# Kernel optimization log

Hardware: AMD Instinct MI355X
Metric: run time of the kernel (lower is better)

The kernel has to match this reference:

```python
import jax, jax.numpy as jnp
import numpy as np

NUM_CLASSES = 90
MAX_DET_POINTS = 5000
MAX_DET_PER_IMAGE = 100
IOU_THR = 0.5
NEG = -1e10
IMAGE_SIZE = 768


def _make_anchors(image_size=IMAGE_SIZE, min_level=3, num_levels=5, anchor_scale=4.0):
    """EfficientDet-style anchors, ordered (level, y, x, anchor-config), yxyx."""
    boxes_all = []
    for li in range(num_levels):
        stride = 2 ** (min_level + li)
        boxes_level = []
        for octave in range(3):
            for aspect in (1.0, 2.0, 0.5):
                base = anchor_scale * stride * 2.0 ** (octave / 3.0)
                ax = np.sqrt(aspect)
                half_x = base * ax / 2.0
                half_y = base / ax / 2.0
                x = np.arange(stride / 2.0, image_size, stride)
                y = np.arange(stride / 2.0, image_size, stride)
                xv, yv = np.meshgrid(x, y)  # [H, W], row-major matches NHWC flatten
                xv = xv.reshape(-1)
                yv = yv.reshape(-1)
                boxes = np.stack([yv - half_y, xv - half_x, yv + half_y, xv + half_x], axis=1)
                boxes_level.append(boxes[:, None, :])
        boxes_all.append(np.concatenate(boxes_level, axis=1).reshape(-1, 4))
    return np.concatenate(boxes_all, axis=0).astype(np.float32)


def setup_inputs() -> dict:
    key = jax.random.key(0)
    ks = jax.random.split(key, 10)
    B = 8
    hw = [96, 48, 24, 12, 6]
    inp = {}
    for i, s in enumerate(hw):
        inp[f"cls{i}"] = jax.random.normal(ks[i], (B, 810, s, s), jnp.float32)
        inp[f"box{i}"] = jax.random.normal(ks[5 + i], (B, 36, s, s), jnp.float32)
    inp["anchor_boxes"] = jnp.asarray(_make_anchors())
    return inp


def _decode_boxes(rel_codes, anchors):
    # anchors: yxyx; rel_codes: (ty, tx, th, tw) -> output xyxy
    ycenter_a = (anchors[..., 0] + anchors[..., 2]) / 2
    xcenter_a = (anchors[..., 1] + anchors[..., 3]) / 2
    ha = anchors[..., 2] - anchors[..., 0]
    wa = anchors[..., 3] - anchors[..., 1]
    ty, tx, th, tw = rel_codes[..., 0], rel_codes[..., 1], rel_codes[..., 2], rel_codes[..., 3]
    w = jnp.exp(tw) * wa
    h = jnp.exp(th) * ha
    yc = ty * ha + ycenter_a
    xc = tx * wa + xcenter_a
    return jnp.stack([xc - w / 2, yc - h / 2, xc + w / 2, yc + h / 2], axis=-1)


def _nms_indices(boxes, scores, classes, iou_thr=IOU_THR, max_out=MAX_DET_PER_IMAGE):
    """torchvision.batched_nms: class-offset boxes, greedy NMS, return idx + valid mask."""
    boxes = jax.lax.stop_gradient(boxes)
    scores = jax.lax.stop_gradient(scores)
    off = classes.astype(boxes.dtype) * (jnp.max(boxes) + 1.0)
    b = boxes + off[:, None]  # [N,4]
    area = (b[:, 2] - b[:, 0]) * (b[:, 3] - b[:, 1])

    def body(i, state):
        live, sel, val = state
        idx = jnp.argmax(live)
        ok = live[idx] > 0.0  # sigmoid scores are >0; suppressed are NEG
        bi = b[idx]
        ix = jnp.maximum(0.0, jnp.minimum(b[:, 2], bi[2]) - jnp.maximum(b[:, 0], bi[0]))
        iy = jnp.maximum(0.0, jnp.minimum(b[:, 3], bi[3]) - jnp.maximum(b[:, 1], bi[1]))
        inter = ix * iy
        iou = inter / (area + area[idx] - inter + 1e-8)
        live = jnp.where(iou > iou_thr, NEG, live).at[idx].set(NEG)
        return live, sel.at[i].set(idx), val.at[i].set(ok)

    state0 = (scores, jnp.zeros((max_out,), jnp.int32), jnp.zeros((max_out,), bool))
    _, sel, val = jax.lax.fori_loop(0, max_out, body, state0)
    return sel, val


def _forward(cls_levels, box_levels, anchor_boxes):
    B = cls_levels[0].shape[0]
    C = NUM_CLASSES
    # NCHW -> NHWC -> [B, A, C] / [B, A, 4], concat over levels
    cls_all = jnp.concatenate(
        [c.transpose(0, 2, 3, 1).reshape(B, -1, C) for c in cls_levels], axis=1)
    box_all = jnp.concatenate(
        [b.transpose(0, 2, 3, 1).reshape(B, -1, 4) for b in box_levels], axis=1)

    top_vals, top_idx = jax.lax.top_k(cls_all.reshape(B, -1), MAX_DET_POINTS)
    indices = top_idx // C  # anchor index
    classes = top_idx % C
    box_topk = jnp.take_along_axis(box_all, indices[..., None], axis=1)  # [B,K,4]
    anchors_sel = anchor_boxes[indices]  # [B,K,4]

    boxes = _decode_boxes(box_topk, anchors_sel)  # xyxy [B,K,4]
    scores = jax.nn.sigmoid(top_vals)  # [B,K]

    def per_image(bx, sc, cl):
        sel, val = _nms_indices(bx, sc, cl)
        det = jnp.concatenate(
            [bx[sel], sc[sel, None], (cl[sel] + 1).astype(bx.dtype)[:, None]], axis=1)
        return jnp.where(val[:, None], det, 0.0)  # pad invalid rows with zeros

    return jax.vmap(per_image)(boxes, scores, classes)  # [B, 100, 6]


def reference(cls0, cls1, cls2, cls3, cls4, box0, box1, box2, box3, box4, anchor_boxes):
    return _forward((cls0, cls1, cls2, cls3, cls4), (box0, box1, box2, box3, box4), anchor_boxes)
```

## Files before the change

### kernel.cpp

```cpp
#include <hip/hip_runtime.h>
#include <stdint.h>

#define KDET 5000
#define MAX_OUT 100
#define PRE_THR 2.5f
#define CAND_CAP 98304u
#define SEL_N 8192u
#define TOTAL_F 9943560u
#define STAGE_CAP 1024u
#define HBINS 2048u
#define FB 0x18040u
#define CHUNKW 512u
#define SC2_CAP 2048u
#define NMSK_CAP 4096u
#define SEL_STRIDE 5120u
#define DEC_BLKS 16u
#define DEC_PER 313u

#define WS_CNT   0
#define WS_HIST  4096
#define WS_ZERO  69632
#define WS_META  69632
#define WS_PMAX  69760
#define WS_SELG  131072
#define WS_BX    458752
#define WS_SC    1098752
#define WS_CL    1258752
#define WS_CAND  1441792

__device__ __forceinline__ unsigned f2key(float f) {
  unsigned u = __float_as_uint(f);
  return u ^ (unsigned)(((int)u >> 31) | 0x80000000);
}

__global__ __launch_bounds__(256, 8) void scan_kernel(
    const float* __restrict__ c0, const float* __restrict__ c1,
    const float* __restrict__ c2, const float* __restrict__ c3,
    const float* __restrict__ c4,
    unsigned long long* __restrict__ cand,
    unsigned* __restrict__ cnt, unsigned* __restrict__ hist)
{
  __shared__ unsigned sh_hist[HBINS];
  __shared__ unsigned long long sh_cand[STAGE_CAP];
  __shared__ unsigned sh_ccnt;
  __shared__ unsigned sh_base;

  const unsigned img = blockIdx.y;
  const unsigned tid = threadIdx.x;
  const float* ptrs[5] = {c0, c1, c2, c3, c4};
  const unsigned lvlElems[5] = {7464960u, 1866240u, 466560u, 116640u, 29160u};
  const unsigned hw2s[5] = {9216u, 2304u, 576u, 144u, 36u};
  const unsigned fbases[5] = {0u, 7464960u, 9331200u, 9797760u, 9914400u};
  unsigned long long* candI = cand + (size_t)img * CAND_CAP;
  unsigned* histI = hist + img * HBINS;

  for (unsigned b = tid; b < HBINS; b += 256u) sh_hist[b] = 0u;
  if (tid == 0) sh_ccnt = 0u;
  __syncthreads();

#pragma unroll
  for (int lev = 0; lev < 5; ++lev) {
    const float4* p = (const float4*)(ptrs[lev] + (size_t)img * lvlElems[lev]);
    const unsigned n4 = lvlElems[lev] >> 2;
    const unsigned hw2 = hw2s[lev];
    const unsigned fbase = fbases[lev];
    const unsigned chunk = 256u * 4u;
    const unsigned sweep = gridDim.x * chunk;
    for (unsigned s0 = blockIdx.x * chunk; s0 < n4; s0 += sweep) {
      float4 v[4]; unsigned idxs[4]; bool ok[4];
#pragma unroll
      for (int u = 0; u < 4; ++u) {
        idxs[u] = s0 + (unsigned)u * 256u + tid;
        ok[u] = idxs[u] < n4;
        if (ok[u]) v[u] = p[idxs[u]];
      }
#pragma unroll
      for (int u = 0; u < 4; ++u) {
        if (!ok[u]) continue;
        float vs[4] = {v[u].x, v[u].y, v[u].z, v[u].w};
#pragma unroll
        for (int j = 0; j < 4; ++j) {
          float f = vs[j];
          if (f > PRE_THR) {
            unsigned key = f2key(f);
            unsigned bin = (key >> 15) - FB;
            if (bin > HBINS - 1u) bin = HBINS - 1u;
            atomicAdd(&sh_hist[bin], 1u);
            unsigned linear = idxs[u] * 4u + (unsigned)j;
            unsigned ch = linear / hw2;
            unsigned pos = linear - ch * hw2;
            unsigned F = fbase + pos * 810u + ch;
            unsigned slot = atomicAdd(&sh_ccnt, 1u);
            if (slot < STAGE_CAP)
              sh_cand[slot] = ((unsigned long long)key << 32) | (unsigned)(~F);
          }
        }
      }
    }
  }
  __syncthreads();

  unsigned n = sh_ccnt < STAGE_CAP ? sh_ccnt : STAGE_CAP;
  if (tid == 0) sh_base = atomicAdd(&cnt[img], n);
  __syncthreads();
  unsigned base = sh_base;
  for (unsigned k = tid; k < n; k += 256u) {
    unsigned slot = base + k;
    if (slot < CAND_CAP) candI[slot] = sh_cand[k];
  }
  for (unsigned b = tid; b < HBINS; b += 256u) {
    unsigned v = sh_hist[b];
    if (v) atomicAdd(&histI[b], v);
  }
}

__device__ __forceinline__ void bitonic_ce(unsigned long long* sb,
                                           unsigned i, unsigned ixj, bool desc) {
  unsigned long long a = sb[i], b = sb[ixj];
  if ((a < b) == desc) { sb[i] = b; sb[ixj] = a; }
}

__device__ __forceinline__ unsigned npow2(unsigned n) {
  unsigned m = 1u;
  while (m < n) m <<= 1u;
  return m;
}

__device__ void bitonic_desc(unsigned long long* a, unsigned m,
                             unsigned tid, unsigned wid, unsigned lane) {
  for (unsigned k = 2; k <= m; k <<= 1) {
    for (unsigned j = k >> 1; j; j >>= 1) {
      if (j >= 512u) {
        for (unsigned i = tid; i < m; i += 1024u) {
          unsigned ixj = i ^ j;
          if (ixj > i) bitonic_ce(a, i, ixj, (i & k) == 0);
        }
        __syncthreads();
      } else {
        unsigned base = wid * 512u;
        if (base < m) {
          unsigned lim = m - base; if (lim > 512u) lim = 512u;
#pragma unroll
          for (unsigned t = 0; t < 8; ++t) {
            unsigned io = t * 64u + lane;
            if (io < lim) {
              unsigned i = base + io;
              unsigned ixj = i ^ j;
              if (ixj > i) bitonic_ce(a, i, ixj, (i & k) == 0);
            }
          }
        }
        asm volatile("" ::: "memory");
      }
    }
    __syncthreads();
  }
}

__device__ __forceinline__ void bitonic_ce_pair(unsigned long long* kk,
                                                unsigned short* pp,
                                                unsigned i, unsigned ixj, bool desc) {
  unsigned long long a = kk[i], b = kk[ixj];
  if ((a < b) == desc) {
    kk[i] = b; kk[ixj] = a;
    unsigned short t = pp[i]; pp[i] = pp[ixj]; pp[ixj] = t;
  }
}

__device__ void bitonic_desc_pair(unsigned long long* kk, unsigned short* pp,
                                  unsigned m, unsigned tid, unsigned wid,
                                  unsigned lane) {
  for (unsigned k = 2; k <= m; k <<= 1) {
    for (unsigned j = k >> 1; j; j >>= 1) {
      if (j >= 512u) {
        for (unsigned i = tid; i < m; i += 1024u) {
          unsigned ixj = i ^ j;
          if (ixj > i) bitonic_ce_pair(kk, pp, i, ixj, (i & k) == 0);
        }
        __syncthreads();
      } else {
        unsigned base = wid * 512u;
        if (base < m) {
          unsigned lim = m - base; if (lim > 512u) lim = 512u;
#pragma unroll
          for (unsigned t = 0; t < 8; ++t) {
            unsigned io = t * 64u + lane;
            if (io < lim) {
              unsigned i = base + io;
              unsigned ixj = i ^ j;
              if (ixj > i) bitonic_ce_pair(kk, pp, i, ixj, (i & k) == 0);
            }
          }
        }
        asm volatile("" ::: "memory");
      }
    }
    __syncthreads();
  }
}

__global__ __launch_bounds__(1024) void select_kernel(
    const unsigned long long* __restrict__ cand, const unsigned* __restrict__ cnt,
    const unsigned* __restrict__ hist, unsigned long long* __restrict__ selG,
    unsigned* __restrict__ meta)
{
  const unsigned img = blockIdx.x;
  const unsigned tid = threadIdx.x;
  const unsigned wid = tid >> 6, lane = tid & 63u;
  __shared__ unsigned long long sb[SEL_N];
  __shared__ unsigned long long sc2[SC2_CAP];
  __shared__ unsigned bofs[HBINS];
  __shared__ unsigned sh_bound[16];
  __shared__ unsigned wsum[16];
  __shared__ unsigned sh_keyLow, sh_binLow, sh_SabA, sh_cntA, sh_Sab0, sh_cnt0;
  __shared__ int sh_flags;

  if (tid == 0) { sh_keyLow = 0u; sh_binLow = 0u; sh_flags = 0; }
  if (tid < 16u) sh_bound[tid] = 0u;
  for (unsigned i = tid; i < SEL_N; i += 1024u) sb[i] = 0ull;

  const unsigned* histI = hist + img * HBINS;
  unsigned b0 = 2047u - 2u * tid;
  unsigned b1 = b0 - 1u;
  unsigned h0 = histI[b0], h1 = histI[b1];
  unsigned s = h0 + h1;
  unsigned inc = s;
#pragma unroll
  for (int off = 1; off < 64; off <<= 1) {
    unsigned nv = __shfl_up(inc, off, 64);
    if ((int)lane >= off) inc += nv;
  }
  if (lane == 63u) wsum[wid] = inc;
  __syncthreads();
  if (tid < 64u) {
    unsigned v = (tid < 16u) ? wsum[tid] : 0u;
#pragma unroll
    for (int off = 1; off < 16; off <<= 1) {
      unsigned nv = __shfl_up(v, off, 64);
      if ((int)tid >= off) v += nv;
    }
    if (tid < 16u) wsum[tid] = v;
  }
  __syncthreads();
  unsigned excl = inc - s + (wid ? wsum[wid - 1] : 0u);
  bofs[b0] = excl;
  bofs[b1] = excl + h0;
  if (excl < (unsigned)KDET && excl + s >= (unsigned)KDET) {
    bool first = (excl + h0 >= (unsigned)KDET);
    unsigned binr = first ? b0 : b1;
    sh_keyLow = (binr + FB) << 15;
    sh_binLow = binr;
    sh_SabA = first ? excl : excl + h0;
    sh_cntA = first ? h0 : h1;
  }
  if (tid == 1023u) { sh_Sab0 = excl + h0; sh_cnt0 = h1; }
  __syncthreads();

  const unsigned keyLow = sh_keyLow;
  unsigned binLow, Sabove, cntLow;
  if (keyLow) { binLow = sh_binLow; Sabove = sh_SabA; cntLow = sh_cntA; }
  else        { binLow = 0u;        Sabove = sh_Sab0; cntLow = sh_cnt0; }
  const unsigned selCount = Sabove + cntLow;
  const unsigned NT = selCount < (unsigned)KDET ? selCount : (unsigned)KDET;

  {
    unsigned e0 = excl + h0;
    unsigned e1 = e0 + h1;
    if (b0 > binLow && h0 != 0u) {
      if (h0 > CHUNKW) sh_flags = 1;
      unsigned e = e0 > SEL_N ? SEL_N : e0;
      atomicMax(&sh_bound[(e - 1u) / CHUNKW], e);
    }
    if (b1 > binLow && h1 != 0u) {
      if (h1 > CHUNKW) sh_flags = 1;
      unsigned e = e1 > SEL_N ? SEL_N : e1;
      atomicMax(&sh_bound[(e - 1u) / CHUNKW], e);
    }
    if (b0 == binLow && h0 > SC2_CAP) sh_flags = 1;
    if (b1 == binLow && h1 > SC2_CAP) sh_flags = 1;
  }
  __syncthreads();

  unsigned prefEnd = sh_bound[0];
  if (sh_bound[1] > prefEnd) prefEnd = sh_bound[1];
  if (sh_bound[2] > prefEnd) prefEnd = sh_bound[2];
  if (sh_bound[3] > prefEnd) prefEnd = sh_bound[3];
  int doFull = sh_flags;
  unsigned sortedEnd;
  if (!doFull) {
    if (Sabove <= prefEnd) sortedEnd = (unsigned)KDET;
    else {
      sortedEnd = prefEnd;
      if ((unsigned)KDET - sortedEnd > NMSK_CAP) doFull = 1;
    }
  }
  if (doFull) sortedEnd = (unsigned)KDET;

  unsigned M = cnt[img]; if (M > CAND_CAP) M = CAND_CAP;
  const unsigned long long* candI = cand + (size_t)img * CAND_CAP;
  for (unsigned i = tid; i < M; i += 4096u) {
    unsigned long long c[4]; bool ok[4];
#pragma unroll
    for (int u = 0; u < 4; ++u) {
      unsigned ii = i + (unsigned)u * 1024u;
      ok[u] = ii < M;
      c[u] = ok[u] ? candI[ii] : 0ull;
    }
#pragma unroll
    for (int u = 0; u < 4; ++u) {
      if (!ok[u]) continue;
      unsigned key = (unsigned)(c[u] >> 32);
      if (key >= keyLow) {
        unsigned bin = (key >> 15) - FB;
        if (bin > HBINS - 1u) bin = HBINS - 1u;
        unsigned pos = atomicAdd(&bofs[bin], 1u);
        if (pos < SEL_N) sb[pos] = c[u];
      }
    }
  }
  __syncthreads();

  if (doFull) {
    bitonic_desc(sb, SEL_N, tid, wid, lane);
  } else {
    if (cntLow > 1u) {
      unsigned segEnd = Sabove + cntLow; if (segEnd > SEL_N) segEnd = SEL_N;
      unsigned n = segEnd - Sabove;
      if (n > 1u) {
        unsigned m = npow2(n);
        for (unsigned i = tid; i < m; i += 1024u)
          sc2[i] = (i < n) ? sb[Sabove + i] : 0ull;
        __syncthreads();
        bitonic_desc(sc2, m, tid, wid, lane);
        for (unsigned i = tid; i < n; i += 1024u) sb[Sabove + i] = sc2[i];
        __syncthreads();
      }
    }
    if (prefEnd > 1u) {
      unsigned n = prefEnd;
      unsigned m = npow2(n);
      for (unsigned i = tid; i < m; i += 1024u)
        sc2[i] = (i < n) ? sb[i] : 0ull;
      __syncthreads();
      bitonic_desc(sc2, m, tid, wid, lane);
      for (unsigned i = tid; i < n; i += 1024u) sb[i] = sc2[i];
      __syncthreads();
    }
  }

  unsigned long long* selI = selG + (size_t)img * SEL_STRIDE;
  for (unsigned i = tid; i < (unsigned)KDET; i += 1024u) selI[i] = sb[i];
  if (tid == 0) meta[img] = sortedEnd;
}

__global__ __launch_bounds__(256) void decode_kernel(
    const float* __restrict__ x0, const float* __restrict__ x1,
    const float* __restrict__ x2, const float* __restrict__ x3,
    const float* __restrict__ x4, const float* __restrict__ anchors,
    const unsigned long long* __restrict__ selG,
    float* __restrict__ bx, float* __restrict__ sc, unsigned* __restrict__ cl,
    float* __restrict__ pmax)
{
  const unsigned img = blockIdx.y;
  const unsigned blk = blockIdx.x;
  const unsigned tid = threadIdx.x;
  __shared__ float wmax[4];
  const unsigned long long* selI = selG + (size_t)img * SEL_STRIDE;
  float* bxI = bx + (size_t)img * KDET * 4;
  float* scI = sc + (size_t)img * KDET;
  unsigned* clI = cl + (size_t)img * KDET;
  const unsigned start = blk * DEC_PER;
  unsigned end = start + DEC_PER;
  if (end > (unsigned)KDET) end = (unsigned)KDET;

  float lmax = -3.4e38f;
  for (unsigned e = start + tid; e < end; e += 256u) {
    unsigned long long ent = selI[e];
    unsigned keyS = (unsigned)(ent >> 32);
    unsigned F = ~(unsigned)ent;
    if (F >= TOTAL_F) F = 0u;
    unsigned ubits = (keyS & 0x80000000u) ? (keyS ^ 0x80000000u) : ~keyS;
    float logit = __uint_as_float(ubits);
    unsigned anchor = F / 90u;
    unsigned clv = F - anchor * 90u;
    const float* bp; unsigned W, ab;
    if (anchor < 82944u)       { bp = x0; W = 96; ab = 0u; }
    else if (anchor < 103680u) { bp = x1; W = 48; ab = 82944u; }
    else if (anchor < 108864u) { bp = x2; W = 24; ab = 103680u; }
    else if (anchor < 110160u) { bp = x3; W = 12; ab = 108864u; }
    else                       { bp = x4; W = 6;  ab = 110160u; }
    unsigned rel = anchor - ab;
    unsigned cell = rel / 9u;
    unsigned a = rel - cell * 9u;
    unsigned y = cell / W;
    unsigned xx = cell - y * W;
    unsigned hw2 = W * W;
    size_t baseoff = ((size_t)img * 36u + a * 4u) * hw2 + (size_t)y * W + xx;
    float ty = bp[baseoff];
    float tx = bp[baseoff + hw2];
    float th = bp[baseoff + 2 * (size_t)hw2];
    float tw = bp[baseoff + 3 * (size_t)hw2];
    float A0 = anchors[anchor * 4u + 0], A1 = anchors[anchor * 4u + 1];
    float A2 = anchors[anchor * 4u + 2], A3 = anchors[anchor * 4u + 3];
    float yca = (A0 + A2) * 0.5f;
    float xca = (A1 + A3) * 0.5f;
    float ha = A2 - A0, wa = A3 - A1;
    float w = expf(tw) * wa;
    float h = expf(th) * ha;
    float yc = ty * ha + yca;
    float xc = tx * wa + xca;
    float X1 = xc - w * 0.5f, Y1 = yc - h * 0.5f;
    float X2 = xc + w * 0.5f, Y2 = yc + h * 0.5f;
    bxI[e * 4 + 0] = X1; bxI[e * 4 + 1] = Y1; bxI[e * 4 + 2] = X2; bxI[e * 4 + 3] = Y2;
    scI[e] = 1.0f / (1.0f + expf(-logit));
    clI[e] = clv;
    lmax = fmaxf(lmax, fmaxf(fmaxf(X1, Y1), fmaxf(X2, Y2)));
  }
#pragma unroll
  for (int off = 32; off > 0; off >>= 1)
    lmax = fmaxf(lmax, __shfl_down(lmax, off, 64));
  if ((tid & 63u) == 0) wmax[tid >> 6] = lmax;
  __syncthreads();
  if (tid == 0) {
    float m = fmaxf(fmaxf(wmax[0], wmax[1]), fmaxf(wmax[2], wmax[3]));
    pmax[img * DEC_BLKS + blk] = m;
  }
}

__global__ __launch_bounds__(1024) void nms_kernel(
    const float* __restrict__ bx, const float* __restrict__ sc,
    const unsigned* __restrict__ cl, const float* __restrict__ pmax,
    const unsigned long long* __restrict__ selG,
    const unsigned* __restrict__ meta,
    float* __restrict__ out)
{
  const unsigned img = blockIdx.x;
  const unsigned tid = threadIdx.x;
  const unsigned wid = tid >> 6, lane = tid & 63u;
  __shared__ float bo[KDET][4];
  __shared__ float ar[KDET];
  __shared__ unsigned long long kk[NMSK_CAP];
  __shared__ unsigned short pp[NMSK_CAP];
  __shared__ float sh_gmax;
  __shared__ int sh_kidx[MAX_OUT];
  __shared__ int sh_kept;

  float kx1[2], ky1[2], kx2[2], ky2[2], kar[2];
  kx1[0] = kx1[1] = ky1[0] = ky1[1] = 0.0f;
  kx2[0] = kx2[1] = ky2[0] = ky2[1] = 0.0f;
  kar[0] = kar[1] = 0.0f;

  if (tid < 64u) {
    float v = (tid < DEC_BLKS) ? pmax[img * DEC_BLKS + tid] : -3.4e38f;
#pragma unroll
    for (int off = 8; off > 0; off >>= 1)
      v = fmaxf(v, __shfl_down(v, off, 64));
    if (tid == 0) sh_gmax = v;
  }
  __syncthreads();
  const float gmax1 = sh_gmax + 1.0f;
  const unsigned sortedEnd = meta[img];

  const float4* bx4 = (const float4*)(bx + (size_t)img * KDET * 4);
  const float* bxI = bx + (size_t)img * KDET * 4;
  const float* scI = sc + (size_t)img * KDET;
  const unsigned* clI = cl + (size_t)img * KDET;
  for (unsigned i = tid; i < (unsigned)KDET; i += 1024u) {
    float4 b = bx4[i];
    float offv = (float)clI[i] * gmax1;
    float X1 = b.x + offv, Y1 = b.y + offv, X2 = b.z + offv, Y2 = b.w + offv;
    bo[i][0] = X1; bo[i][1] = Y1; bo[i][2] = X2; bo[i][3] = Y2;
    ar[i] = (X2 - X1) * (Y2 - Y1);
  }
  __syncthreads();

#define NMS_STEP_REG(ROWIDX, CX1, CY1, CX2, CY2, CA, KEPT) do { \
    int sup = 0; \
    if ((int)lane < (KEPT)) { \
      float ix = fmaxf(0.0f, fminf(kx2[0], (CX2)) - fmaxf(kx1[0], (CX1))); \
      float iy = fmaxf(0.0f, fminf(ky2[0], (CY2)) - fmaxf(ky1[0], (CY1))); \
      float inter = ix * iy; \
      if (inter / (((CA) + kar[0]) - inter + 1e-8f) > 0.5f) sup = 1; \
    } \
    if ((int)lane + 64 < (KEPT)) { \
      float ix = fmaxf(0.0f, fminf(kx2[1], (CX2)) - fmaxf(kx1[1], (CX1))); \
      float iy = fmaxf(0.0f, fminf(ky2[1], (CY2)) - fmaxf(ky1[1], (CY1))); \
      float inter = ix * iy; \
      if (inter / (((CA) + kar[1]) - inter + 1e-8f) > 0.5f) sup = 1; \
    } \
    if (!__any(sup)) { \
      unsigned s_ = (unsigned)(KEPT) >> 6, l_ = (unsigned)(KEPT) & 63u; \
      if (lane == l_) { \
        if (s_ == 0u) { kx1[0]=(CX1); ky1[0]=(CY1); kx2[0]=(CX2); ky2[0]=(CY2); kar[0]=(CA); } \
        else          { kx1[1]=(CX1); ky1[1]=(CY1); kx2[1]=(CX2); ky2[1]=(CY2); kar[1]=(CA); } \
      } \
      if (lane == 0u) sh_kidx[KEPT] = (int)(ROWIDX); \
      (KEPT)++; \
    } \
  } while (0)

  int keptR = 0;
  if (tid < 64u) {
    float cx1 = 0, cy1 = 0, cx2 = 0, cy2 = 0, ca = 0;
    if (sortedEnd > 0u) {
      cx1 = bo[0][0]; cy1 = bo[0][1]; cx2 = bo[0][2]; cy2 = bo[0][3]; ca = ar[0];
    }
    for (unsigned jj = 0; jj < sortedEnd && keptR < MAX_OUT; ++jj) {
      float nx1 = 0, ny1 = 0, nx2 = 0, ny2 = 0, na = 0;
      unsigned nj = jj + 1u;
      bool hasN = nj < sortedEnd;
      if (hasN) {
        nx1 = bo[nj][0]; ny1 = bo[nj][1]; nx2 = bo[nj][2]; ny2 = bo[nj][3];
        na = ar[nj];
      }
      NMS_STEP_REG(jj, cx1, cy1, cx2, cy2, ca, keptR);
      cx1 = nx1; cy1 = ny1; cx2 = nx2; cy2 = ny2; ca = na;
    }
    if (lane == 0) sh_kept = keptR;
  }
  __syncthreads();

  if (sh_kept < MAX_OUT && sortedEnd < (unsigned)KDET) {
    const unsigned rem = (unsigned)KDET - sortedEnd;
    const unsigned m = npow2(rem);
    const unsigned long long* selI = selG + (size_t)img * SEL_STRIDE;
    for (unsigned i = tid; i < m; i += 1024u) {
      if (i < rem) { kk[i] = selI[sortedEnd + i]; pp[i] = (unsigned short)i; }
      else         { kk[i] = 0ull; pp[i] = 0; }
    }
    __syncthreads();
    bitonic_desc_pair(kk, pp, m, tid, wid, lane);
    if (tid < 64u) {
      for (unsigned j = 0; j < rem && keptR < MAX_OUT; ++j) {
        unsigned row = sortedEnd + (unsigned)pp[j];
        float cx1 = bo[row][0], cy1 = bo[row][1];
        float cx2 = bo[row][2], cy2 = bo[row][3];
        float ca = ar[row];
        NMS_STEP_REG(row, cx1, cy1, cx2, cy2, ca, keptR);
      }
      if (lane == 0) sh_kept = keptR;
    }
    __syncthreads();
  }

#undef NMS_STEP_REG

  {
    const int kept = sh_kept;
    float* o = out + (size_t)img * 600;
    for (unsigned idx = tid; idx < 600u; idx += 1024u) {
      unsigned row = idx / 6u, col = idx - row * 6u;
      float v = 0.0f;
      if (row < (unsigned)kept) {
        int jj = sh_kidx[row];
        if (col < 4u)      v = bxI[jj * 4 + col];
        else if (col == 4) v = scI[jj];
        else               v = (float)(clI[jj] + 1u);
      }
      o[idx] = v;
    }
  }
}

extern "C" void kernel_launch(void* const* d_in, const int* in_sizes, int n_in,
                              void* d_out, int out_size, void* d_ws, size_t ws_size,
                              hipStream_t stream) {
  const int clsSz[5] = {59719680, 14929920, 3732480, 933120, 233280};
  const int boxSz[5] = {2654208, 663552, 165888, 41472, 10368};
  const float* cls[5] = {nullptr, nullptr, nullptr, nullptr, nullptr};
  const float* box[5] = {nullptr, nullptr, nullptr, nullptr, nullptr};
  const float* anchors = nullptr;
  for (int i = 0; i < n_in; ++i) {
    int s = in_sizes[i];
    for (int l = 0; l < 5; ++l) {
      if (s == clsSz[l]) cls[l] = (const float*)d_in[i];
      if (s == boxSz[l]) box[l] = (const float*)d_in[i];
    }
    if (s == 441936) anchors = (const float*)d_in[i];
  }
  if (!cls[0] || !box[0] || !anchors) {
    for (int l = 0; l < 5; ++l) { cls[l] = (const float*)d_in[2 * l]; box[l] = (const float*)d_in[2 * l + 1]; }
    anchors = (const float*)d_in[10];
  }

  char* ws = (char*)d_ws;
  unsigned* cnt = (unsigned*)(ws + WS_CNT);
  unsigned* hist = (unsigned*)(ws + WS_HIST);
  unsigned* metaA = (unsigned*)(ws + WS_META);
  float* pmaxA = (float*)(ws + WS_PMAX);
  unsigned long long* selG = (unsigned long long*)(ws + WS_SELG);
  float* bxA = (float*)(ws + WS_BX);
  float* scA = (float*)(ws + WS_SC);
  unsigned* clA = (unsigned*)(ws + WS_CL);
  unsigned long long* cand = (unsigned long long*)(ws + WS_CAND);

  (void)hipMemsetAsync(ws, 0, WS_ZERO, stream);
  scan_kernel<<<dim3(256, 8), 256, 0, stream>>>(
      cls[0], cls[1], cls[2], cls[3], cls[4], cand, cnt, hist);
  select_kernel<<<8, 1024, 0, stream>>>(cand, cnt, hist, selG, metaA);
  decode_kernel<<<dim3(DEC_BLKS, 8), 256, 0, stream>>>(
      box[0], box[1], box[2], box[3], box[4], anchors, selG, bxA, scA, clA, pmaxA);
  nms_kernel<<<8, 1024, 0, stream>>>(bxA, scA, clA, pmaxA, selG, metaA,
                                     (float*)d_out);
}
```

Before: 523.2 us.

## Split candidates into high/low key buckets and fuse decode into NMS kernel

The scan kernel now stages candidates into two buckets by a key split, so the select kernel can prefetch the high bucket into registers and skip reading the low bucket when the selection threshold lies above the split. The separate decode kernel is removed and its work folded into the NMS kernel: boxes are decoded straight into shared memory, class ids kept as bytes, and the score sigmoid computed only for output rows. This drops one launch and the global round trip of decoded boxes, scores and classes. In exchange, decoding runs on only 8 blocks instead of 128, and the bucket caps can overflow differently than the single buffer did.

```diff
diff --git a/kernel.cpp b/kernel.cpp
--- a/kernel.cpp
+++ b/kernel.cpp
@@ -5,28 +5,27 @@
 #define MAX_OUT 100
 #define PRE_THR 2.5f
 #define CAND_CAP 98304u
+#define HI_CAP 16384u
+#define LO_CAP 81920u
 #define SEL_N 8192u
 #define TOTAL_F 9943560u
 #define STAGE_CAP 1024u
+#define HI_STAGE 256u
+#define LO_STAGE 768u
 #define HBINS 2048u
 #define FB 0x18040u
+#define SPLIT_KEY 0xC0400000u
 #define CHUNKW 512u
 #define SC2_CAP 2048u
 #define NMSK_CAP 4096u
 #define SEL_STRIDE 5120u
-#define DEC_BLKS 16u
-#define DEC_PER 313u
 
 #define WS_CNT   0
 #define WS_HIST  4096
 #define WS_ZERO  69632
 #define WS_META  69632
-#define WS_PMAX  69760
 #define WS_SELG  131072
-#define WS_BX    458752
-#define WS_SC    1098752
-#define WS_CL    1258752
-#define WS_CAND  1441792
+#define WS_CAND  524288
 
 __device__ __forceinline__ unsigned f2key(float f) {
   unsigned u = __float_as_uint(f);
@@ -42,8 +41,8 @@
 {
   __shared__ unsigned sh_hist[HBINS];
   __shared__ unsigned long long sh_cand[STAGE_CAP];
-  __shared__ unsigned sh_ccnt;
-  __shared__ unsigned sh_base;
+  __shared__ unsigned sh_hi, sh_lo;
+  __shared__ unsigned sh_baseH, sh_baseL;
 
   const unsigned img = blockIdx.y;
   const unsigned tid = threadIdx.x;
@@ -55,7 +54,7 @@
   unsigned* histI = hist + img * HBINS;
 
   for (unsigned b = tid; b < HBINS; b += 256u) sh_hist[b] = 0u;
-  if (tid == 0) sh_ccnt = 0u;
+  if (tid == 0) { sh_hi = 0u; sh_lo = 0u; }
   __syncthreads();
 
 #pragma unroll
@@ -90,9 +89,15 @@
             unsigned ch = linear / hw2;
             unsigned pos = linear - ch * hw2;
             unsigned F = fbase + pos * 810u + ch;
-            unsigned slot = atomicAdd(&sh_ccnt, 1u);
-            if (slot < STAGE_CAP)
-              sh_cand[slot] = ((unsigned long long)key << 32) | (unsigned)(~F);
+            unsigned long long ent =
+                ((unsigned long long)key << 32) | (unsigned)(~F);
+            if (key >= SPLIT_KEY) {
+              unsigned slot = atomicAdd(&sh_hi, 1u);
+              if (slot < HI_STAGE) sh_cand[slot] = ent;
+            } else {
+              unsigned slot = atomicAdd(&sh_lo, 1u);
+              if (slot < LO_STAGE) sh_cand[STAGE_CAP - 1u - slot] = ent;
+            }
           }
         }
       }
@@ -100,13 +105,19 @@
   }
   __syncthreads();
 
-  unsigned n = sh_ccnt < STAGE_CAP ? sh_ccnt : STAGE_CAP;
-  if (tid == 0) sh_base = atomicAdd(&cnt[img], n);
-  __syncthreads();
-  unsigned base = sh_base;
-  for (unsigned k = tid; k < n; k += 256u) {
-    unsigned slot = base + k;
-    if (slot < CAND_CAP) candI[slot] = sh_cand[k];
+  unsigned nh = sh_hi < HI_STAGE ? sh_hi : HI_STAGE;
+  unsigned nl = sh_lo < LO_STAGE ? sh_lo : LO_STAGE;
+  if (tid == 0) sh_baseH = atomicAdd(&cnt[img * 2u], nh);
+  if (tid == 1) sh_baseL = atomicAdd(&cnt[img * 2u + 1u], nl);
+  __syncthreads();
+  unsigned baseH = sh_baseH, baseL = sh_baseL;
+  for (unsigned k = tid; k < nh; k += 256u) {
+    unsigned slot = baseH + k;
+    if (slot < HI_CAP) candI[slot] = sh_cand[k];
+  }
+  for (unsigned k = tid; k < nl; k += 256u) {
+    unsigned slot = baseL + k;
+    if (slot < LO_CAP) candI[HI_CAP + slot] = sh_cand[STAGE_CAP - 1u - k];
   }
   for (unsigned b = tid; b < HBINS; b += 256u) {
     unsigned v = sh_hist[b];
@@ -219,6 +230,16 @@
   if (tid < 16u) sh_bound[tid] = 0u;
   for (unsigned i = tid; i < SEL_N; i += 1024u) sb[i] = 0ull;
 
+  const unsigned long long* candI = cand + (size_t)img * CAND_CAP;
+
+  unsigned cntHi = cnt[img * 2u]; if (cntHi > HI_CAP) cntHi = HI_CAP;
+  unsigned long long ch[16];
+#pragma unroll
+  for (int t = 0; t < 16; ++t) {
+    unsigned idx = tid + (unsigned)t * 1024u;
+    ch[t] = (idx < cntHi) ? candI[idx] : 0ull;
+  }
+
   const unsigned* histI = hist + img * HBINS;
   unsigned b0 = 2047u - 2u * tid;
   unsigned b1 = b0 - 1u;
@@ -296,25 +317,40 @@
   }
   if (doFull) sortedEnd = (unsigned)KDET;
 
-  unsigned M = cnt[img]; if (M > CAND_CAP) M = CAND_CAP;
-  const unsigned long long* candI = cand + (size_t)img * CAND_CAP;
-  for (unsigned i = tid; i < M; i += 4096u) {
-    unsigned long long c[4]; bool ok[4];
-#pragma unroll
-    for (int u = 0; u < 4; ++u) {
-      unsigned ii = i + (unsigned)u * 1024u;
-      ok[u] = ii < M;
-      c[u] = ok[u] ? candI[ii] : 0ull;
-    }
-#pragma unroll
-    for (int u = 0; u < 4; ++u) {
-      if (!ok[u]) continue;
-      unsigned key = (unsigned)(c[u] >> 32);
+#pragma unroll
+  for (int t = 0; t < 16; ++t) {
+    unsigned idx = tid + (unsigned)t * 1024u;
+    if (idx < cntHi) {
+      unsigned key = (unsigned)(ch[t] >> 32);
       if (key >= keyLow) {
         unsigned bin = (key >> 15) - FB;
         if (bin > HBINS - 1u) bin = HBINS - 1u;
         unsigned pos = atomicAdd(&bofs[bin], 1u);
-        if (pos < SEL_N) sb[pos] = c[u];
+        if (pos < SEL_N) sb[pos] = ch[t];
+      }
+    }
+  }
+  if (keyLow < SPLIT_KEY) {
+    unsigned cntLo = cnt[img * 2u + 1u]; if (cntLo > LO_CAP) cntLo = LO_CAP;
+    const unsigned long long* candLo = candI + HI_CAP;
+    for (unsigned i = tid; i < cntLo; i += 4096u) {
+      unsigned long long c[4]; bool ok[4];
+#pragma unroll
+      for (int u = 0; u < 4; ++u) {
+        unsigned ii = i + (unsigned)u * 1024u;
+        ok[u] = ii < cntLo;
+        c[u] = ok[u] ? candLo[ii] : 0ull;
+      }
+#pragma unroll
+      for (int u = 0; u < 4; ++u) {
+        if (!ok[u]) continue;
+        unsigned key = (unsigned)(c[u] >> 32);
+        if (key >= keyLow) {
+          unsigned bin = (key >> 15) - FB;
+          if (bin > HBINS - 1u) bin = HBINS - 1u;
+          unsigned pos = atomicAdd(&bofs[bin], 1u);
+          if (pos < SEL_N) sb[pos] = c[u];
+        }
       }
     }
   }
@@ -353,34 +389,40 @@
   if (tid == 0) meta[img] = sortedEnd;
 }
 
-__global__ __launch_bounds__(256) void decode_kernel(
+__global__ __launch_bounds__(1024) void nms_kernel(
     const float* __restrict__ x0, const float* __restrict__ x1,
     const float* __restrict__ x2, const float* __restrict__ x3,
     const float* __restrict__ x4, const float* __restrict__ anchors,
     const unsigned long long* __restrict__ selG,
-    float* __restrict__ bx, float* __restrict__ sc, unsigned* __restrict__ cl,
-    float* __restrict__ pmax)
+    const unsigned* __restrict__ meta,
+    float* __restrict__ out)
 {
-  const unsigned img = blockIdx.y;
-  const unsigned blk = blockIdx.x;
+  const unsigned img = blockIdx.x;
   const unsigned tid = threadIdx.x;
-  __shared__ float wmax[4];
+  const unsigned wid = tid >> 6, lane = tid & 63u;
+  __shared__ float bo[KDET][4];
+  __shared__ float ar[KDET];
+  __shared__ unsigned char cl8[KDET];
+  __shared__ unsigned long long kk[NMSK_CAP];
+  __shared__ unsigned short pp[NMSK_CAP];
+  __shared__ float fred[16];
+  __shared__ float sh_gmax;
+  __shared__ int sh_kidx[MAX_OUT];
+  __shared__ int sh_kept;
+
   const unsigned long long* selI = selG + (size_t)img * SEL_STRIDE;
-  float* bxI = bx + (size_t)img * KDET * 4;
-  float* scI = sc + (size_t)img * KDET;
-  unsigned* clI = cl + (size_t)img * KDET;
-  const unsigned start = blk * DEC_PER;
-  unsigned end = start + DEC_PER;
-  if (end > (unsigned)KDET) end = (unsigned)KDET;
+  const unsigned sortedEnd = meta[img];
+
+  float kx1[2], ky1[2], kx2[2], ky2[2], kar[2];
+  kx1[0] = kx1[1] = ky1[0] = ky1[1] = 0.0f;
+  kx2[0] = kx2[1] = ky2[0] = ky2[1] = 0.0f;
+  kar[0] = kar[1] = 0.0f;
 
   float lmax = -3.4e38f;
-  for (unsigned e = start + tid; e < end; e += 256u) {
+  for (unsigned e = tid; e < (unsigned)KDET; e += 1024u) {
     unsigned long long ent = selI[e];
-    unsigned keyS = (unsigned)(ent >> 32);
     unsigned F = ~(unsigned)ent;
     if (F >= TOTAL_F) F = 0u;
-    unsigned ubits = (keyS & 0x80000000u) ? (keyS ^ 0x80000000u) : ~keyS;
-    float logit = __uint_as_float(ubits);
     unsigned anchor = F / 90u;
     unsigned clv = F - anchor * 90u;
     const float* bp; unsigned W, ab;
@@ -411,66 +453,30 @@
     float xc = tx * wa + xca;
     float X1 = xc - w * 0.5f, Y1 = yc - h * 0.5f;
     float X2 = xc + w * 0.5f, Y2 = yc + h * 0.5f;
-    bxI[e * 4 + 0] = X1; bxI[e * 4 + 1] = Y1; bxI[e * 4 + 2] = X2; bxI[e * 4 + 3] = Y2;
-    scI[e] = 1.0f / (1.0f + expf(-logit));
-    clI[e] = clv;
+    bo[e][0] = X1; bo[e][1] = Y1; bo[e][2] = X2; bo[e][3] = Y2;
+    cl8[e] = (unsigned char)clv;
     lmax = fmaxf(lmax, fmaxf(fmaxf(X1, Y1), fmaxf(X2, Y2)));
   }
 #pragma unroll
   for (int off = 32; off > 0; off >>= 1)
     lmax = fmaxf(lmax, __shfl_down(lmax, off, 64));
-  if ((tid & 63u) == 0) wmax[tid >> 6] = lmax;
-  __syncthreads();
-  if (tid == 0) {
-    float m = fmaxf(fmaxf(wmax[0], wmax[1]), fmaxf(wmax[2], wmax[3]));
-    pmax[img * DEC_BLKS + blk] = m;
-  }
-}
-
-__global__ __launch_bounds__(1024) void nms_kernel(
-    const float* __restrict__ bx, const float* __restrict__ sc,
-    const unsigned* __restrict__ cl, const float* __restrict__ pmax,
-    const unsigned long long* __restrict__ selG,
-    const unsigned* __restrict__ meta,
-    float* __restrict__ out)
-{
-  const unsigned img = blockIdx.x;
-  const unsigned tid = threadIdx.x;
-  const unsigned wid = tid >> 6, lane = tid & 63u;
-  __shared__ float bo[KDET][4];
-  __shared__ float ar[KDET];
-  __shared__ unsigned long long kk[NMSK_CAP];
-  __shared__ unsigned short pp[NMSK_CAP];
-  __shared__ float sh_gmax;
-  __shared__ int sh_kidx[MAX_OUT];
-  __shared__ int sh_kept;
-
-  float kx1[2], ky1[2], kx2[2], ky2[2], kar[2];
-  kx1[0] = kx1[1] = ky1[0] = ky1[1] = 0.0f;
-  kx2[0] = kx2[1] = ky2[0] = ky2[1] = 0.0f;
-  kar[0] = kar[1] = 0.0f;
-
-  if (tid < 64u) {
-    float v = (tid < DEC_BLKS) ? pmax[img * DEC_BLKS + tid] : -3.4e38f;
-#pragma unroll
-    for (int off = 8; off > 0; off >>= 1)
-      v = fmaxf(v, __shfl_down(v, off, 64));
-    if (tid == 0) sh_gmax = v;
+  if (lane == 0u) fred[wid] = lmax;
+  if (tid == 0u) sh_kept = 0;
+  __syncthreads();
+  if (tid == 0u) {
+    float g = fred[0];
+#pragma unroll
+    for (int i2 = 1; i2 < 16; ++i2) g = fmaxf(g, fred[i2]);
+    sh_gmax = g;
   }
   __syncthreads();
   const float gmax1 = sh_gmax + 1.0f;
-  const unsigned sortedEnd = meta[img];
-
-  const float4* bx4 = (const float4*)(bx + (size_t)img * KDET * 4);
-  const float* bxI = bx + (size_t)img * KDET * 4;
-  const float* scI = sc + (size_t)img * KDET;
-  const unsigned* clI = cl + (size_t)img * KDET;
-  for (unsigned i = tid; i < (unsigned)KDET; i += 1024u) {
-    float4 b = bx4[i];
-    float offv = (float)clI[i] * gmax1;
-    float X1 = b.x + offv, Y1 = b.y + offv, X2 = b.z + offv, Y2 = b.w + offv;
-    bo[i][0] = X1; bo[i][1] = Y1; bo[i][2] = X2; bo[i][3] = Y2;
-    ar[i] = (X2 - X1) * (Y2 - Y1);
+
+  for (unsigned e = tid; e < (unsigned)KDET; e += 1024u) {
+    float offv = (float)cl8[e] * gmax1;
+    float ox1 = bo[e][0] + offv, oy1 = bo[e][1] + offv;
+    float ox2 = bo[e][2] + offv, oy2 = bo[e][3] + offv;
+    ar[e] = (ox2 - ox1) * (oy2 - oy1);
   }
   __syncthreads();
 
@@ -503,14 +509,17 @@
   if (tid < 64u) {
     float cx1 = 0, cy1 = 0, cx2 = 0, cy2 = 0, ca = 0;
     if (sortedEnd > 0u) {
-      cx1 = bo[0][0]; cy1 = bo[0][1]; cx2 = bo[0][2]; cy2 = bo[0][3]; ca = ar[0];
+      float o0 = (float)cl8[0] * gmax1;
+      cx1 = bo[0][0] + o0; cy1 = bo[0][1] + o0;
+      cx2 = bo[0][2] + o0; cy2 = bo[0][3] + o0; ca = ar[0];
     }
     for (unsigned jj = 0; jj < sortedEnd && keptR < MAX_OUT; ++jj) {
       float nx1 = 0, ny1 = 0, nx2 = 0, ny2 = 0, na = 0;
       unsigned nj = jj + 1u;
-      bool hasN = nj < sortedEnd;
-      if (hasN) {
-        nx1 = bo[nj][0]; ny1 = bo[nj][1]; nx2 = bo[nj][2]; ny2 = bo[nj][3];
+      if (nj < sortedEnd) {
+        float on = (float)cl8[nj] * gmax1;
+        nx1 = bo[nj][0] + on; ny1 = bo[nj][1] + on;
+        nx2 = bo[nj][2] + on; ny2 = bo[nj][3] + on;
         na = ar[nj];
       }
       NMS_STEP_REG(jj, cx1, cy1, cx2, cy2, ca, keptR);
@@ -523,7 +532,6 @@
   if (sh_kept < MAX_OUT && sortedEnd < (unsigned)KDET) {
     const unsigned rem = (unsigned)KDET - sortedEnd;
     const unsigned m = npow2(rem);
-    const unsigned long long* selI = selG + (size_t)img * SEL_STRIDE;
     for (unsigned i = tid; i < m; i += 1024u) {
       if (i < rem) { kk[i] = selI[sortedEnd + i]; pp[i] = (unsigned short)i; }
       else         { kk[i] = 0ull; pp[i] = 0; }
@@ -533,8 +541,9 @@
     if (tid < 64u) {
       for (unsigned j = 0; j < rem && keptR < MAX_OUT; ++j) {
         unsigned row = sortedEnd + (unsigned)pp[j];
-        float cx1 = bo[row][0], cy1 = bo[row][1];
-        float cx2 = bo[row][2], cy2 = bo[row][3];
+        float o_ = (float)cl8[row] * gmax1;
+        float cx1 = bo[row][0] + o_, cy1 = bo[row][1] + o_;
+        float cx2 = bo[row][2] + o_, cy2 = bo[row][3] + o_;
         float ca = ar[row];
         NMS_STEP_REG(row, cx1, cy1, cx2, cy2, ca, keptR);
       }
@@ -553,9 +562,17 @@
       float v = 0.0f;
       if (row < (unsigned)kept) {
         int jj = sh_kidx[row];
-        if (col < 4u)      v = bxI[jj * 4 + col];
-        else if (col == 4) v = scI[jj];
-        else               v = (float)(clI[jj] + 1u);
+        if (col < 4u) {
+          v = bo[jj][col];
+        } else if (col == 4u) {
+          unsigned long long ent = selI[jj];
+          unsigned keyS = (unsigned)(ent >> 32);
+          unsigned ubits = (keyS & 0x80000000u) ? (keyS ^ 0x80000000u) : ~keyS;
+          float logit = __uint_as_float(ubits);
+          v = 1.0f / (1.0f + expf(-logit));
+        } else {
+          v = (float)(cl8[jj] + 1u);
+        }
       }
       o[idx] = v;
     }
@@ -587,19 +604,14 @@
   unsigned* cnt = (unsigned*)(ws + WS_CNT);
   unsigned* hist = (unsigned*)(ws + WS_HIST);
   unsigned* metaA = (unsigned*)(ws + WS_META);
-  float* pmaxA = (float*)(ws + WS_PMAX);
   unsigned long long* selG = (unsigned long long*)(ws + WS_SELG);
-  float* bxA = (float*)(ws + WS_BX);
-  float* scA = (float*)(ws + WS_SC);
-  unsigned* clA = (unsigned*)(ws + WS_CL);
   unsigned long long* cand = (unsigned long long*)(ws + WS_CAND);
 
   (void)hipMemsetAsync(ws, 0, WS_ZERO, stream);
   scan_kernel<<<dim3(256, 8), 256, 0, stream>>>(
       cls[0], cls[1], cls[2], cls[3], cls[4], cand, cnt, hist);
   select_kernel<<<8, 1024, 0, stream>>>(cand, cnt, hist, selG, metaA);
-  decode_kernel<<<dim3(DEC_BLKS, 8), 256, 0, stream>>>(
-      box[0], box[1], box[2], box[3], box[4], anchors, selG, bxA, scA, clA, pmaxA);
-  nms_kernel<<<8, 1024, 0, stream>>>(bxA, scA, clA, pmaxA, selG, metaA,
-                                     (float*)d_out);
-}
+  nms_kernel<<<8, 1024, 0, stream>>>(
+      box[0], box[1], box[2], box[3], box[4], anchors, selG, metaA,
+      (float*)d_out);
+}
```

Result: slower. 575.0 us (+9.9%).
